# Kernel optimization log

Hardware: AMD Instinct MI355X
Metric: run time of the kernel (lower is better)

Reference implementation:

```python
import jax, jax.numpy as jnp
import numpy as np

EPS = 1e-6
LAM = 0.005


def setup_inputs() -> dict:
    key = jax.random.key(0)
    k1, k2, k3 = jax.random.split(key, 3)
    B, D, H, W, M = 16, 256, 128, 128, 4096
    z = jax.random.normal(k1, (B, D, H, W), dtype=jnp.float32)
    z_prime = jax.random.normal(k2, (B, D, H, W), dtype=jnp.float32)
    # Precomputed sampled pixel indices (flat over H*W). With randn inputs every
    # pixel passes the validity mask, so uniform sampling matches the original.
    flat_idx = jax.random.randint(k3, (B, M), 0, H * W, dtype=jnp.int32)
    return {"z": z, "z_prime": z_prime, "flat_idx": flat_idx}


def _gather_pixels(z, flat_idx):
    # z: (B, D, H, W), flat_idx: (B, M) -> (B*M, D)
    B, D, H, W = z.shape
    M = flat_idx.shape[1]
    z_flat = z.reshape(B, D, H * W)
    g = jnp.take_along_axis(z_flat, flat_idx[:, None, :], axis=2)  # (B, D, M)
    return g.transpose(0, 2, 1).reshape(B * M, D)


def _normalise(x):
    mean = jnp.mean(x, axis=0, keepdims=True)
    std = jnp.std(x, axis=0, keepdims=True, ddof=1)  # torch .std() is unbiased
    return (x - mean) / jnp.clip(std, EPS, None)


def reference(z, z_prime, flat_idx):
    D = z.shape[1]
    zm = _normalise(_gather_pixels(z, flat_idx))        # (N, D)
    zpm = _normalise(_gather_pixels(z_prime, flat_idx))  # (N, D)
    N = zm.shape[0]
    C = (zm.T @ zpm) / N                                 # (D, D)
    on_diag = jnp.diagonal(C)
    off_diag = C.reshape(-1)[1:].reshape(D - 1, D + 1)[:, :-1]
    loss = jnp.sum((1.0 - on_diag) ** 2) + LAM * jnp.sum(off_diag ** 2)
    return loss
```

## Files before the change

### kernel.cpp

```cpp
#include <hip/hip_runtime.h>
#include <hip/hip_bf16.h>

typedef short s16x8 __attribute__((ext_vector_type(8)));
typedef float f32x16 __attribute__((ext_vector_type(16)));

namespace {
constexpr int kB = 16;
constexpr int kD = 256;
constexpr int kHW = 16384;
constexpr int kM = 4096;
constexpr int kN = kB * kM;
constexpr int kWin = 1024;
constexpr int kNWin = kHW / kWin;
constexpr int kNBlk = kB * kNWin;
constexpr int kKT = 16;
constexpr int kNIter = kWin / kKT;
constexpr float kLam = 0.005f;

constexpr int kLdsRing = 32768;
constexpr int kLdsFrag = 98304;
constexpr int kLdsCnt  = 131072;
constexpr int kLdsTot  = 135168;

__device__ __forceinline__ unsigned short f2bf(float f) {
    union { float f; unsigned u; } x{f};
    const unsigned r = x.u + 0x7FFFu + ((x.u >> 16) & 1u);
    return (unsigned short)(r >> 16);
}
__device__ __forceinline__ float bf2f(unsigned short h) {
    union { unsigned u; float f; } x;
    x.u = ((unsigned)h) << 16;
    return x.f;
}
}

__global__ __launch_bounds__(256) void count_kernel(
    const int* __restrict__ flat_idx, int* __restrict__ cnt)
{
    __shared__ int h[kHW];
    const int t = threadIdx.x;
    const int b = blockIdx.x;
    for (int i = t; i < kHW; i += 256) h[i] = 0;
    __syncthreads();
    const int* bi = flat_idx + b * kM;
    for (int i = t; i < kM; i += 256) atomicAdd(&h[bi[i]], 1);
    __syncthreads();
    int* dst = cnt + b * kHW;
    for (int i = t; i < kHW; i += 256) dst[i] = h[i];
}

__global__ __launch_bounds__(512) void fused_gram_kernel(
    const float* __restrict__ z, const float* __restrict__ zp,
    const int* __restrict__ cnt,
    __hip_bfloat16* __restrict__ partial, float* __restrict__ statsPart)
{
    __shared__ char smem[kLdsTot];

    const int bx = blockIdx.x;
    const int b = bx & (kB - 1);
    const int win0 = (bx >> 4) * kWin;
    const int t = threadIdx.x;
    const int w = t >> 6, lane = t & 63, l31 = lane & 31, half = lane >> 5;
    const int wr = w >> 2;
    const int wc = w & 3;
    const int rbase = t >> 2;
    const int cg = t & 3;

    const float* zb  = z  + (size_t)b * kD * kHW;
    const float* zpb = zp + (size_t)b * kD * kHW;
    const int* cb = cnt + b * kHW + win0;

    f32x16 acc[4][2];
#pragma unroll
    for (int i = 0; i < 4; ++i)
#pragma unroll
        for (int j = 0; j < 2; ++j)
#pragma unroll
            for (int r = 0; r < 16; ++r) acc[i][j][r] = 0.f;

    float sA[2], ssA[2], sB[2], ssB[2];
#pragma unroll
    for (int q = 0; q < 2; ++q) { sA[q] = ssA[q] = sB[q] = ssB[q] = 0.f; }

    auto STAGE_CNT = [&]() {
#pragma unroll
        for (int j = 0; j < 2; ++j) {
            const int inst = 2 * w + j;
            const int* gp = cb + inst * 64 + lane;
            __builtin_amdgcn_global_load_lds(
                (const __attribute__((address_space(1))) void*)gp,
                (__attribute__((address_space(3))) void*)(smem + kLdsCnt + inst * 256),
                4, 0, 0);
        }
    };

    auto STAGE = [&](int kt) {
        char* slot = smem + (kt % 3) * kLdsRing;
        const int colb = win0 + kt * kKT + (lane & 3) * 4;
#pragma unroll
        for (int j = 0; j < 2; ++j) {
            const int c = 2 * w + j;
            const int row = 16 * c + (lane >> 2);
            const float* gpA = zb  + (size_t)row * kHW + colb;
            const float* gpB = zpb + (size_t)row * kHW + colb;
            __builtin_amdgcn_global_load_lds(
                (const __attribute__((address_space(1))) void*)gpA,
                (__attribute__((address_space(3))) void*)(slot + c * 1024), 16, 0, 0);
            __builtin_amdgcn_global_load_lds(
                (const __attribute__((address_space(1))) void*)gpB,
                (__attribute__((address_space(3))) void*)(slot + 16384 + c * 1024), 16, 0, 0);
        }
    };

    auto CONV = [&](int kt) {
        const char* Af = smem + (kt % 3) * kLdsRing;
        const char* Bf = Af + 16384;
        char* Ad = smem + kLdsFrag + (kt & 1) * 16384;
        char* Bd = Ad + 8192;
        const int4 ci = *(const int4*)(smem + kLdsCnt + ((kt * 16 + cg * 4) << 2));
        const float cf[4] = {(float)ci.x, (float)ci.y, (float)ci.z, (float)ci.w};
#pragma unroll
        for (int q = 0; q < 2; ++q) {
            const int row = rbase + 128 * q;
            const float4 va = *(const float4*)(Af + row * 64 + cg * 16);
            const float4 vb = *(const float4*)(Bf + row * 64 + cg * 16);
            const float a[4]  = {va.x, va.y, va.z, va.w};
            const float bb[4] = {vb.x, vb.y, vb.z, vb.w};
            ushort4 pa, pb;
            unsigned short* pav = (unsigned short*)&pa;
            unsigned short* pbv = (unsigned short*)&pb;
#pragma unroll
            for (int j = 0; j < 4; ++j) {
                const float wbv = cf[j] * bb[j];
                sA[q]  = fmaf(cf[j], a[j], sA[q]);
                ssA[q] = fmaf(cf[j], a[j] * a[j], ssA[q]);
                sB[q]  = fmaf(cf[j], bb[j], sB[q]);
                ssB[q] = fmaf(cf[j], bb[j] * bb[j], ssB[q]);
                pav[j] = f2bf(a[j]);
                pbv[j] = f2bf(wbv);
            }
            const int off = (((cg >> 1) * 256 + row) << 4) + ((cg & 1) << 3);
            *(unsigned long long*)(Ad + off) = *(unsigned long long*)&pa;
            *(unsigned long long*)(Bd + off) = *(unsigned long long*)&pb;
        }
    };

    auto MFMA_STEP = [&](int fb) {
        const char* As = smem + kLdsFrag + fb * 16384;
        const char* Bs = As + 8192;
        s16x8 af[4], bfr[2];
#pragma unroll
        for (int rt = 0; rt < 4; ++rt) {
            const int row = 128 * wr + 32 * rt + l31;
            af[rt] = *(const s16x8*)(As + ((half * 256 + row) << 4));
        }
#pragma unroll
        for (int ct = 0; ct < 2; ++ct) {
            const int row = 64 * wc + 32 * ct + l31;
            bfr[ct] = *(const s16x8*)(Bs + ((half * 256 + row) << 4));
        }
#pragma unroll
        for (int rt = 0; rt < 4; ++rt)
#pragma unroll
            for (int ct = 0; ct < 2; ++ct)
                acc[rt][ct] = __builtin_amdgcn_mfma_f32_32x32x16_bf16(
                    af[rt], bfr[ct], acc[rt][ct], 0, 0, 0);
    };

    STAGE_CNT();
    STAGE(0);
    asm volatile("s_waitcnt vmcnt(0)" ::: "memory");
    __builtin_amdgcn_s_barrier();
    __builtin_amdgcn_sched_barrier(0);
    CONV(0);
    STAGE(1);
    STAGE(2);
    asm volatile("s_waitcnt lgkmcnt(0)" ::: "memory");
    __builtin_amdgcn_s_barrier();

    for (int kt = 0; kt < kNIter; ++kt) {
        if (kt <= kNIter - 3) asm volatile("s_waitcnt vmcnt(4)" ::: "memory");
        else                  asm volatile("s_waitcnt vmcnt(0)" ::: "memory");
        __builtin_amdgcn_s_barrier();
        __builtin_amdgcn_sched_barrier(0);
        if (kt + 3 < kNIter) STAGE(kt + 3);
        if (kt + 1 < kNIter) CONV(kt + 1);
        MFMA_STEP(kt & 1);
        asm volatile("s_waitcnt lgkmcnt(0)" ::: "memory");
        __builtin_amdgcn_s_barrier();
    }
    __syncthreads();

    __hip_bfloat16* out = partial + (size_t)bx * (kD * kD);
#pragma unroll
    for (int rt = 0; rt < 4; ++rt)
#pragma unroll
        for (int ct = 0; ct < 2; ++ct)
#pragma unroll
            for (int r = 0; r < 16; ++r) {
                const int row = 128 * wr + 32 * rt + (r & 3) + 8 * (r >> 2) + 4 * half;
                const int col = 64 * wc + 32 * ct + l31;
                ((unsigned short*)out)[row * kD + col] = f2bf(acc[rt][ct][r]);
            }

    float* sd = (float*)smem;
#pragma unroll
    for (int q = 0; q < 2; ++q) {
        const int row = rbase + 128 * q;
        float* p = sd + (row * 4 + cg) * 4;
        p[0] = sA[q]; p[1] = ssA[q]; p[2] = sB[q]; p[3] = ssB[q];
    }
    __syncthreads();
    {
        const int row = t >> 1;
        const int pair = t & 1;
        float a0 = 0.f, a1 = 0.f;
#pragma unroll
        for (int g = 0; g < 4; ++g) {
            a0 += sd[(row * 4 + g) * 4 + 2 * pair];
            a1 += sd[(row * 4 + g) * 4 + 2 * pair + 1];
        }
        float* p = statsPart + ((size_t)bx * kD + row) * 4;
        p[2 * pair] = a0;
        p[2 * pair + 1] = a1;
    }
}

__global__ __launch_bounds__(256) void reduce_gram_kernel(
    const __hip_bfloat16* __restrict__ partial, const float* __restrict__ statsPart,
    float* __restrict__ G, float* __restrict__ statsRed)
{
    const int d = blockIdx.x;
    const int t = threadIdx.x;
    const int eg = t & 31;
    const int cgp = t >> 5;

    float fa[8];
#pragma unroll
    for (int j = 0; j < 8; ++j) fa[j] = 0.f;
    const unsigned short* pbase = (const unsigned short*)partial + d * kD + eg * 8;
    for (int c0 = 0; c0 < kNBlk / 8; ++c0) {
        const int c = c0 * 8 + cgp;
        const s16x8 v = *(const s16x8*)(pbase + (size_t)c * (kD * kD));
#pragma unroll
        for (int j = 0; j < 8; ++j)
            fa[j] += bf2f(((const unsigned short*)&v)[j]);
    }
    __shared__ float sd[8][256];
#pragma unroll
    for (int j = 0; j < 8; ++j) sd[cgp][eg * 8 + j] = fa[j];
    __syncthreads();
    {
        const int e = t;
        float s = 0.f;
#pragma unroll
        for (int g = 0; g < 8; ++g) s += sd[g][e];
        G[d * kD + e] = s;
    }

    float x0 = 0.f, x1 = 0.f, x2 = 0.f, x3 = 0.f;
    if (t < kNBlk) {
        const float4 v = *(const float4*)(statsPart + ((size_t)t * kD + d) * 4);
        x0 = v.x; x1 = v.y; x2 = v.z; x3 = v.w;
    }
#pragma unroll
    for (int o = 32; o; o >>= 1) {
        x0 += __shfl_down(x0, o);
        x1 += __shfl_down(x1, o);
        x2 += __shfl_down(x2, o);
        x3 += __shfl_down(x3, o);
    }
    __shared__ float r[4][4];
    if ((t & 63) == 0) {
        r[t >> 6][0] = x0; r[t >> 6][1] = x1;
        r[t >> 6][2] = x2; r[t >> 6][3] = x3;
    }
    __syncthreads();
    if (t < 4) {
        statsRed[d * 4 + t] = r[0][t] + r[1][t] + r[2][t] + r[3][t];
    }
}

__global__ __launch_bounds__(256) void loss_kernel(
    const float* __restrict__ G, const float* __restrict__ statsRed,
    float* __restrict__ out)
{
    __shared__ float muA[kD], isA[kD], muB[kD], isB[kD];
    const int t = threadIdx.x;
    const float4 v = *(const float4*)(statsRed + t * 4);
    const float n = (float)kN;
    const float mA = v.x / n, mB = v.z / n;
    const float vA = (v.y - n * mA * mA) / (n - 1.f);
    const float vB = (v.w - n * mB * mB) / (n - 1.f);
    const float sdA = fmaxf(sqrtf(fmaxf(vA, 0.f)), 1e-6f);
    const float sdB = fmaxf(sqrtf(fmaxf(vB, 0.f)), 1e-6f);
    muA[t] = mA; isA[t] = 1.f / sdA;
    muB[t] = mB; isB[t] = 1.f / sdB;
    __syncthreads();

    float acc = 0.f;
    for (int d = 0; d < kD; ++d) {
        const int e = t;
        const float c = (G[d * kD + e] / n - muA[d] * muB[e]) * isA[d] * isB[e];
        if (d == e) { const float u = 1.f - c; acc += u * u; }
        else        { acc += kLam * c * c; }
    }
#pragma unroll
    for (int o = 32; o; o >>= 1) acc += __shfl_down(acc, o);
    __shared__ float r[4];
    if ((t & 63) == 0) r[t >> 6] = acc;
    __syncthreads();
    if (t == 0) out[0] = r[0] + r[1] + r[2] + r[3];
}

extern "C" void kernel_launch(void* const* d_in, const int* in_sizes, int n_in,
                              void* d_out, int out_size, void* d_ws, size_t ws_size,
                              hipStream_t stream) {
    const float* z  = (const float*)d_in[0];
    const float* zp = (const float*)d_in[1];
    const int* flat_idx = (const int*)d_in[2];
    float* out = (float*)d_out;

    char* ws = (char*)d_ws;
    int* cnt = (int*)ws;
    float* statsPart = (float*)(ws + (size_t)1 * 1024 * 1024);
    float* statsRed  = (float*)(ws + (size_t)3 * 1024 * 1024);
    float* G = (float*)(ws + (size_t)3 * 1024 * 1024 + 64 * 1024);
    __hip_bfloat16* partial = (__hip_bfloat16*)(ws + (size_t)16 * 1024 * 1024);

    count_kernel<<<kB, 256, 0, stream>>>(flat_idx, cnt);
    fused_gram_kernel<<<kNBlk, 512, 0, stream>>>(z, zp, cnt, partial, statsPart);
    reduce_gram_kernel<<<kD, 256, 0, stream>>>(partial, statsPart, G, statsRed);
    loss_kernel<<<1, 256, 0, stream>>>(G, statsRed, out);
}
```

Before: 200.2 us.

## Replace async 3-stage LDS ring with synchronous 128-wide K tiles and swizzled layout

Drops the global_load_lds triple-buffered pipeline with 16-column steps and instead loads 128-column tiles directly into registers, converts to bf16, and writes them to an XOR-swizzled LDS layout. A second pass reads the tile back, accumulates count-weighted statistics, and rewrites the weighted B tile, then eight MFMA k-steps run per tile. This cuts the number of barrier-separated iterations and aims to avoid LDS bank conflicts. The cost is the loss of load/compute overlap, since global loads are now synchronous before each barrier, plus an extra LDS round trip for the weighting. Statistics are now computed from bf16-rounded values, which lowers their precision.

```diff
diff --git a/kernel.cpp b/kernel.cpp
--- a/kernel.cpp
+++ b/kernel.cpp
@@ -13,14 +13,15 @@
 constexpr int kWin = 1024;
 constexpr int kNWin = kHW / kWin;
 constexpr int kNBlk = kB * kNWin;
-constexpr int kKT = 16;
+constexpr int kKT = 128;
 constexpr int kNIter = kWin / kKT;
 constexpr float kLam = 0.005f;
 
-constexpr int kLdsRing = 32768;
-constexpr int kLdsFrag = 98304;
-constexpr int kLdsCnt  = 131072;
-constexpr int kLdsTot  = 135168;
+constexpr int kAo  = 0;
+constexpr int kBo  = 65536;
+constexpr int kCo  = 131072;
+constexpr int kSo  = 131584;
+constexpr int kTot = 139776;
 
 __device__ __forceinline__ unsigned short f2bf(float f) {
     union { float f; unsigned u; } x{f};
@@ -31,6 +32,9 @@
     union { unsigned u; float f; } x;
     x.u = ((unsigned)h) << 16;
     return x.f;
+}
+__device__ __forceinline__ int ldsOff(int row, int c) {
+    return row * 256 + (((c >> 3) ^ (row & 15)) << 4) + ((c & 7) << 1);
 }
 }
 
@@ -54,7 +58,7 @@
     const int* __restrict__ cnt,
     __hip_bfloat16* __restrict__ partial, float* __restrict__ statsPart)
 {
-    __shared__ char smem[kLdsTot];
+    __shared__ char smem[kTot];
 
     const int bx = blockIdx.x;
     const int b = bx & (kB - 1);
@@ -63,8 +67,12 @@
     const int w = t >> 6, lane = t & 63, l31 = lane & 31, half = lane >> 5;
     const int wr = w >> 2;
     const int wc = w & 3;
-    const int rbase = t >> 2;
-    const int cg = t & 3;
+
+    const int sc0 = (t & 31) * 4;
+    const int skg = sc0 >> 3;
+    const int swoff = (t & 1) << 3;
+    const int crow = t >> 1;
+    const int chalf = (t & 1) * 64;
 
     const float* zb  = z  + (size_t)b * kD * kHW;
     const float* zpb = zp + (size_t)b * kD * kHW;
@@ -78,118 +86,85 @@
 #pragma unroll
             for (int r = 0; r < 16; ++r) acc[i][j][r] = 0.f;
 
-    float sA[2], ssA[2], sB[2], ssB[2];
-#pragma unroll
-    for (int q = 0; q < 2; ++q) { sA[q] = ssA[q] = sB[q] = ssB[q] = 0.f; }
-
-    auto STAGE_CNT = [&]() {
-#pragma unroll
-        for (int j = 0; j < 2; ++j) {
-            const int inst = 2 * w + j;
-            const int* gp = cb + inst * 64 + lane;
-            __builtin_amdgcn_global_load_lds(
-                (const __attribute__((address_space(1))) void*)gp,
-                (__attribute__((address_space(3))) void*)(smem + kLdsCnt + inst * 256),
-                4, 0, 0);
-        }
-    };
-
-    auto STAGE = [&](int kt) {
-        char* slot = smem + (kt % 3) * kLdsRing;
-        const int colb = win0 + kt * kKT + (lane & 3) * 4;
-#pragma unroll
-        for (int j = 0; j < 2; ++j) {
-            const int c = 2 * w + j;
-            const int row = 16 * c + (lane >> 2);
-            const float* gpA = zb  + (size_t)row * kHW + colb;
-            const float* gpB = zpb + (size_t)row * kHW + colb;
-            __builtin_amdgcn_global_load_lds(
-                (const __attribute__((address_space(1))) void*)gpA,
-                (__attribute__((address_space(3))) void*)(slot + c * 1024), 16, 0, 0);
-            __builtin_amdgcn_global_load_lds(
-                (const __attribute__((address_space(1))) void*)gpB,
-                (__attribute__((address_space(3))) void*)(slot + 16384 + c * 1024), 16, 0, 0);
-        }
-    };
-
-    auto CONV = [&](int kt) {
-        const char* Af = smem + (kt % 3) * kLdsRing;
-        const char* Bf = Af + 16384;
-        char* Ad = smem + kLdsFrag + (kt & 1) * 16384;
-        char* Bd = Ad + 8192;
-        const int4 ci = *(const int4*)(smem + kLdsCnt + ((kt * 16 + cg * 4) << 2));
-        const float cf[4] = {(float)ci.x, (float)ci.y, (float)ci.z, (float)ci.w};
-#pragma unroll
-        for (int q = 0; q < 2; ++q) {
-            const int row = rbase + 128 * q;
-            const float4 va = *(const float4*)(Af + row * 64 + cg * 16);
-            const float4 vb = *(const float4*)(Bf + row * 64 + cg * 16);
-            const float a[4]  = {va.x, va.y, va.z, va.w};
-            const float bb[4] = {vb.x, vb.y, vb.z, vb.w};
+    float sA = 0.f, ssA = 0.f, sB = 0.f, ssB = 0.f;
+
+    for (int kt = 0; kt < kNIter; ++kt) {
+        if (t < 32) {
+            const int4 ci = *(const int4*)(cb + kt * kKT + t * 4);
+            const float4 cf = {(float)ci.x, (float)ci.y, (float)ci.z, (float)ci.w};
+            *(float4*)(smem + kCo + t * 16) = cf;
+        }
+        const int gbase = win0 + kt * kKT + sc0;
+#pragma unroll 4
+        for (int p = 0; p < 16; ++p) {
+            const int row = 16 * p + (t >> 5);
+            const float4 va = *(const float4*)(zb  + (size_t)row * kHW + gbase);
+            const float4 vb = *(const float4*)(zpb + (size_t)row * kHW + gbase);
             ushort4 pa, pb;
             unsigned short* pav = (unsigned short*)&pa;
             unsigned short* pbv = (unsigned short*)&pb;
-#pragma unroll
-            for (int j = 0; j < 4; ++j) {
-                const float wbv = cf[j] * bb[j];
-                sA[q]  = fmaf(cf[j], a[j], sA[q]);
-                ssA[q] = fmaf(cf[j], a[j] * a[j], ssA[q]);
-                sB[q]  = fmaf(cf[j], bb[j], sB[q]);
-                ssB[q] = fmaf(cf[j], bb[j] * bb[j], ssB[q]);
-                pav[j] = f2bf(a[j]);
-                pbv[j] = f2bf(wbv);
+            pav[0] = f2bf(va.x); pav[1] = f2bf(va.y);
+            pav[2] = f2bf(va.z); pav[3] = f2bf(va.w);
+            pbv[0] = f2bf(vb.x); pbv[1] = f2bf(vb.y);
+            pbv[2] = f2bf(vb.z); pbv[3] = f2bf(vb.w);
+            const int addr = row * 256 + ((skg ^ (row & 15)) << 4) + swoff;
+            *(unsigned long long*)(smem + kAo + addr) = *(unsigned long long*)&pa;
+            *(unsigned long long*)(smem + kBo + addr) = *(unsigned long long*)&pb;
+        }
+        __syncthreads();
+
+#pragma unroll
+        for (int g = 0; g < 8; ++g) {
+            const int c = chalf + g * 8;
+            const int addr = crow * 256 + (((c >> 3) ^ (crow & 15)) << 4);
+            s16x8 ar = *(const s16x8*)(smem + kAo + addr);
+            s16x8 br = *(const s16x8*)(smem + kBo + addr);
+            const float4 cf0 = *(const float4*)(smem + kCo + c * 4);
+            const float4 cf1 = *(const float4*)(smem + kCo + c * 4 + 16);
+            const float cfv[8] = {cf0.x, cf0.y, cf0.z, cf0.w,
+                                  cf1.x, cf1.y, cf1.z, cf1.w};
+            s16x8 bw;
+            unsigned short* arv = (unsigned short*)&ar;
+            unsigned short* brv = (unsigned short*)&br;
+            unsigned short* bwv = (unsigned short*)&bw;
+#pragma unroll
+            for (int j = 0; j < 8; ++j) {
+                const float a  = bf2f(arv[j]);
+                const float bb = bf2f(brv[j]);
+                const float cf = cfv[j];
+                sA  = fmaf(cf, a, sA);
+                ssA = fmaf(cf * a, a, ssA);
+                sB  = fmaf(cf, bb, sB);
+                ssB = fmaf(cf * bb, bb, ssB);
+                bwv[j] = f2bf(cf * bb);
             }
-            const int off = (((cg >> 1) * 256 + row) << 4) + ((cg & 1) << 3);
-            *(unsigned long long*)(Ad + off) = *(unsigned long long*)&pa;
-            *(unsigned long long*)(Bd + off) = *(unsigned long long*)&pb;
-        }
-    };
-
-    auto MFMA_STEP = [&](int fb) {
-        const char* As = smem + kLdsFrag + fb * 16384;
-        const char* Bs = As + 8192;
-        s16x8 af[4], bfr[2];
-#pragma unroll
-        for (int rt = 0; rt < 4; ++rt) {
-            const int row = 128 * wr + 32 * rt + l31;
-            af[rt] = *(const s16x8*)(As + ((half * 256 + row) << 4));
-        }
-#pragma unroll
-        for (int ct = 0; ct < 2; ++ct) {
-            const int row = 64 * wc + 32 * ct + l31;
-            bfr[ct] = *(const s16x8*)(Bs + ((half * 256 + row) << 4));
-        }
-#pragma unroll
-        for (int rt = 0; rt < 4; ++rt)
-#pragma unroll
-            for (int ct = 0; ct < 2; ++ct)
-                acc[rt][ct] = __builtin_amdgcn_mfma_f32_32x32x16_bf16(
-                    af[rt], bfr[ct], acc[rt][ct], 0, 0, 0);
-    };
-
-    STAGE_CNT();
-    STAGE(0);
-    asm volatile("s_waitcnt vmcnt(0)" ::: "memory");
-    __builtin_amdgcn_s_barrier();
-    __builtin_amdgcn_sched_barrier(0);
-    CONV(0);
-    STAGE(1);
-    STAGE(2);
-    asm volatile("s_waitcnt lgkmcnt(0)" ::: "memory");
-    __builtin_amdgcn_s_barrier();
-
-    for (int kt = 0; kt < kNIter; ++kt) {
-        if (kt <= kNIter - 3) asm volatile("s_waitcnt vmcnt(4)" ::: "memory");
-        else                  asm volatile("s_waitcnt vmcnt(0)" ::: "memory");
-        __builtin_amdgcn_s_barrier();
-        __builtin_amdgcn_sched_barrier(0);
-        if (kt + 3 < kNIter) STAGE(kt + 3);
-        if (kt + 1 < kNIter) CONV(kt + 1);
-        MFMA_STEP(kt & 1);
-        asm volatile("s_waitcnt lgkmcnt(0)" ::: "memory");
-        __builtin_amdgcn_s_barrier();
-    }
-    __syncthreads();
+            *(s16x8*)(smem + kBo + addr) = bw;
+        }
+        __syncthreads();
+
+#pragma unroll
+        for (int ks = 0; ks < 8; ++ks) {
+            const int kg = 2 * ks + half;
+            s16x8 af[4], bfr[2];
+#pragma unroll
+            for (int rt = 0; rt < 4; ++rt) {
+                const int row = 128 * wr + 32 * rt + l31;
+                af[rt] = *(const s16x8*)(smem + kAo + row * 256 + ((kg ^ (row & 15)) << 4));
+            }
+#pragma unroll
+            for (int ct = 0; ct < 2; ++ct) {
+                const int row = 64 * wc + 32 * ct + l31;
+                bfr[ct] = *(const s16x8*)(smem + kBo + row * 256 + ((kg ^ (row & 15)) << 4));
+            }
+#pragma unroll
+            for (int rt = 0; rt < 4; ++rt)
+#pragma unroll
+                for (int ct = 0; ct < 2; ++ct)
+                    acc[rt][ct] = __builtin_amdgcn_mfma_f32_32x32x16_bf16(
+                        af[rt], bfr[ct], acc[rt][ct], 0, 0, 0);
+        }
+        __syncthreads();
+    }
 
     __hip_bfloat16* out = partial + (size_t)bx * (kD * kD);
 #pragma unroll
@@ -203,26 +178,17 @@
                 ((unsigned short*)out)[row * kD + col] = f2bf(acc[rt][ct][r]);
             }
 
-    float* sd = (float*)smem;
-#pragma unroll
-    for (int q = 0; q < 2; ++q) {
-        const int row = rbase + 128 * q;
-        float* p = sd + (row * 4 + cg) * 4;
-        p[0] = sA[q]; p[1] = ssA[q]; p[2] = sB[q]; p[3] = ssB[q];
-    }
-    __syncthreads();
     {
-        const int row = t >> 1;
-        const int pair = t & 1;
-        float a0 = 0.f, a1 = 0.f;
-#pragma unroll
-        for (int g = 0; g < 4; ++g) {
-            a0 += sd[(row * 4 + g) * 4 + 2 * pair];
-            a1 += sd[(row * 4 + g) * 4 + 2 * pair + 1];
-        }
-        float* p = statsPart + ((size_t)bx * kD + row) * 4;
-        p[2 * pair] = a0;
-        p[2 * pair + 1] = a1;
+        float* sd = (float*)(smem + kSo);
+        float* p = sd + (crow * 2 + (t & 1)) * 4;
+        p[0] = sA; p[1] = ssA; p[2] = sB; p[3] = ssB;
+        __syncthreads();
+        if (t < kD) {
+            const float4 v0 = *(const float4*)(sd + (t * 2 + 0) * 4);
+            const float4 v1 = *(const float4*)(sd + (t * 2 + 1) * 4);
+            float4 v = {v0.x + v1.x, v0.y + v1.y, v0.z + v1.z, v0.w + v1.w};
+            *(float4*)(statsPart + ((size_t)bx * kD + t) * 4) = v;
+        }
     }
 }
 
```

Measured after the change: 205.4 us. 2.6% more time.
